# Kernel optimization log

Hardware: AMD Instinct MI355X
Metric: run time of the kernel (lower is better)

## Reference

```python
import jax, jax.numpy as jnp
import numpy as np

N = 50000      # total nodes
E = 800000     # total edges
G = 1000       # graphs in batch
H = 128        # in_channels == hidden_channels
L = 3          # num GCN layers
C = 6          # num classes
EPS = 1e-5     # BatchNorm eps


def setup_inputs() -> dict:
    key = jax.random.key(0)
    ks = jax.random.split(key, 8)
    x = jax.random.normal(ks[0], (N, H), jnp.float32)
    edge_index = jax.random.randint(ks[1], (2, E), 0, N)
    batch = jnp.sort(jax.random.randint(ks[2], (N,), 0, G))
    conv_w = jax.random.normal(ks[3], (L, H, H), jnp.float32) * 0.05
    conv_b = jnp.zeros((L, H), jnp.float32)
    bn_g = jnp.ones((L, H), jnp.float32)
    bn_b = jnp.zeros((L, H), jnp.float32)
    mlp_w1 = jax.random.normal(ks[4], (H, H), jnp.float32) * 0.05
    mlp_b1 = jnp.zeros((H,), jnp.float32)
    mlp_w2 = jax.random.normal(ks[5], (H, C), jnp.float32) * 0.05
    mlp_b2 = jnp.zeros((C,), jnp.float32)
    return {"x": x, "edge_index": edge_index, "batch": batch,
            "conv_w": conv_w, "conv_b": conv_b, "bn_g": bn_g, "bn_b": bn_b,
            "mlp_w1": mlp_w1, "mlp_b1": mlp_b1, "mlp_w2": mlp_w2, "mlp_b2": mlp_b2}


def reference(x, edge_index, batch, conv_w, conv_b, bn_g, bn_b, mlp_w1, mlp_b1, mlp_w2, mlp_b2):
    src, dst = edge_index[0], edge_index[1]
    # GCN symmetric norm with self-loops: deg over A+I
    deg = jax.ops.segment_sum(jnp.ones((E,), x.dtype), dst, num_segments=N) + 1.0
    dis = jax.lax.rsqrt(deg)                      # deg^{-1/2}, [N]
    edge_norm = (dis[src] * dis[dst])[:, None]    # [E,1]
    self_norm = (dis * dis)[:, None]              # [N,1] self-loop weight 1/deg

    for l in range(L):
        h = x @ conv_w[l]                                             # [N,H]
        agg = jax.ops.segment_sum(h[src] * edge_norm, dst, num_segments=N)
        h = agg + h * self_norm + conv_b[l]
        # BatchNorm (training-mode batch statistics, biased var)
        mu = jnp.mean(h, axis=0)
        var = jnp.var(h, axis=0)
        hn = (h - mu) * jax.lax.rsqrt(var + EPS)
        x = jax.nn.relu(hn * bn_g[l] + bn_b[l])   # dropout = identity (eval)

    # global mean pool per graph
    sums = jax.ops.segment_sum(x, batch, num_segments=G)              # [G,H]
    cnt = jax.ops.segment_sum(jnp.ones((N,), x.dtype), batch, num_segments=G)
    pooled = sums / jnp.maximum(cnt, 1.0)[:, None]

    h = jax.nn.relu(pooled @ mlp_w1 + mlp_b1)
    return h @ mlp_w2 + mlp_b2                                         # [G,C]
```

## Files before the change

kernel.cpp:

```cpp
#include <hip/hip_runtime.h>

#define Nn 50000
#define Ee 800000
#define Gg 1000
#define Hh 128
#define Cc 6
#define EPSf 1e-5f
#define SB 1024
#define NSB ((Nn + SB - 1) / SB)
#define NBH 64
#define EPB (Ee / NBH)
#define NW (Nn / 2)
#define HWH (NW / 2)
#define GT ((Nn + 63) / 64)

typedef unsigned short u16;
typedef unsigned int u32;
typedef __attribute__((ext_vector_type(8))) short bf16x8;
typedef __attribute__((ext_vector_type(4))) float f32x4;
typedef __attribute__((ext_vector_type(4))) unsigned int u32x4;

static __device__ inline u16 f2bf(float f) {
    u32 u = __float_as_uint(f);
    u32 r = (u + 0x7fffu + ((u >> 16) & 1u)) >> 16;
    return (u16)r;
}
static __device__ inline float bf_lo(u32 v) { return __uint_as_float(v << 16); }
static __device__ inline float bf_hi(u32 v) { return __uint_as_float(v & 0xffff0000u); }
static __device__ inline u32 pack2(float a, float b) {
    return ((u32)f2bf(b) << 16) | (u32)f2bf(a);
}

__global__ __launch_bounds__(256) void k_pre(const float* __restrict__ W3,
                                             u16* __restrict__ WT3,
                                             float* __restrict__ stats3) {
    __shared__ u16 tbuf[Hh * 136];
    int l = blockIdx.x;
    int tid = threadIdx.x;
    stats3[l * 256 + tid] = 0.0f;
    const float* W = W3 + l * Hh * Hh;
    u16* WT = WT3 + l * Hh * Hh;
#pragma unroll
    for (int i = 0; i < 16; i++) {
        int v = tid + 256 * i;
        int r = v >> 5, c4 = v & 31;
        float4 d = ((const float4*)W)[v];
        u16* p = tbuf + r * 136 + c4 * 4;
        p[0] = f2bf(d.x); p[1] = f2bf(d.y); p[2] = f2bf(d.z); p[3] = f2bf(d.w);
    }
    __syncthreads();
#pragma unroll
    for (int i = 0; i < 64; i++) {
        int o = tid + 256 * i;
        int n = o >> 7, k = o & 127;
        WT[o] = tbuf[k * 136 + n];
    }
}

__global__ __launch_bounds__(256) void k_pro(const int* __restrict__ ei_dst,
                                             u16* __restrict__ rankL,
                                             u32* __restrict__ partials,
                                             const float* __restrict__ Xf,
                                             const u16* __restrict__ WT0,
                                             u16* __restrict__ Yh) {
    extern __shared__ __align__(16) unsigned char smem[];
    int bid = blockIdx.x, tid = threadIdx.x;

    if (bid < NBH) {
        u32* h = (u32*)smem;
        int e0 = bid * EPB;
        u32* P = partials + bid * NW;
#pragma unroll 1
        for (int half = 0; half < 2; half++) {
            int wlo = half * HWH;
            for (int i = tid; i < HWH; i += 256) h[i] = 0u;
            __syncthreads();
            for (int i = tid; i < EPB; i += 256) {
                int d = ei_dst[e0 + i];
                int w = d >> 1;
                if (w >= wlo && w < wlo + HWH) {
                    u32 old = atomicAdd(&h[w - wlo], (d & 1) ? 65536u : 1u);
                    rankL[e0 + i] = (u16)((d & 1) ? (old >> 16) : (old & 0xffffu));
                }
            }
            __syncthreads();
            for (int i = tid; i < HWH; i += 256) P[wlo + i] = h[i];
            __syncthreads();
        }
        return;
    }

    u16* wt = (u16*)smem;
#pragma unroll
    for (int i = 0; i < 8; i++) {
        int v = tid + 256 * i;
        int n = v >> 4, k8 = v & 15;
        uint4 d = ((const uint4*)WT0)[v];
        *((uint4*)(wt + n * 136 + k8 * 8)) = d;
    }
    __syncthreads();

    int tile = bid - NBH;
    int wv = tid >> 6, lane = tid & 63;
    int m = lane & 15, q = lane >> 4;
    int row0 = tile * 64 + wv * 16;
    int lrow = row0 + m;
    if (lrow >= Nn) lrow = Nn - 1;
    const float* xfrow = Xf + lrow * Hh + q * 8;

    f32x4 acc[8] = {};
#pragma unroll
    for (int k0 = 0; k0 < Hh; k0 += 32) {
        float4 u0 = *(const float4*)(xfrow + k0);
        float4 u1 = *(const float4*)(xfrow + k0 + 4);
        union { bf16x8 v; u32 u[4]; } cv;
        cv.u[0] = pack2(u0.x, u0.y);
        cv.u[1] = pack2(u0.z, u0.w);
        cv.u[2] = pack2(u1.x, u1.y);
        cv.u[3] = pack2(u1.z, u1.w);
        bf16x8 a = cv.v;
#pragma unroll
        for (int t = 0; t < 8; t++) {
            bf16x8 b = *(const bf16x8*)(wt + (t * 16 + m) * 136 + k0 + q * 8);
            acc[t] = __builtin_amdgcn_mfma_f32_16x16x32_bf16(a, b, acc[t], 0, 0, 0);
        }
    }

    int orow0 = row0 + q * 4;
#pragma unroll
    for (int t = 0; t < 8; t++) {
#pragma unroll
        for (int r = 0; r < 4; r++) {
            int rr = orow0 + r;
            if (rr < Nn) Yh[rr * Hh + t * 16 + m] = f2bf(acc[t][r]);
        }
    }
}

__global__ __launch_bounds__(256) void k_scan1(const u32* __restrict__ partials,
                                               u32* __restrict__ base_off,
                                               int* __restrict__ rs,
                                               int* __restrict__ bsum,
                                               float* __restrict__ dis,
                                               const int* __restrict__ batch,
                                               int* __restrict__ gstart) {
    __shared__ int ts[256];
    int b = blockIdx.x;
    int t = threadIdx.x;
    int base = b * SB + t * 4;
    int v[4] = {0, 0, 0, 0};
    if (base < Nn) {
        int w0 = base >> 1;
        u32 run0 = 0, run1 = 0;
#pragma unroll 8
        for (int b2 = 0; b2 < NBH; b2++) {
            u32 p0 = partials[b2 * NW + w0];
            u32 p1 = partials[b2 * NW + w0 + 1];
            base_off[b2 * NW + w0] = run0;
            base_off[b2 * NW + w0 + 1] = run1;
            run0 += p0; run1 += p1;
        }
        v[0] = (int)(run0 & 0xffffu); v[1] = (int)(run0 >> 16);
        v[2] = (int)(run1 & 0xffffu); v[3] = (int)(run1 >> 16);
        dis[base]     = rsqrtf((float)v[0] + 1.0f);
        dis[base + 1] = rsqrtf((float)v[1] + 1.0f);
        dis[base + 2] = rsqrtf((float)v[2] + 1.0f);
        dis[base + 3] = rsqrtf((float)v[3] + 1.0f);
    }
    int g = b * 256 + t;
    if (g <= Gg) {
        int lo = 0, hi = Nn;
        while (lo < hi) {
            int mid = (lo + hi) >> 1;
            if (batch[mid] < g) lo = mid + 1; else hi = mid;
        }
        gstart[g] = lo;
    }
    int tsum = v[0] + v[1] + v[2] + v[3];
    ts[t] = tsum;
    __syncthreads();
    for (int off = 1; off < 256; off <<= 1) {
        int x = (t >= off) ? ts[t - off] : 0;
        __syncthreads();
        ts[t] += x;
        __syncthreads();
    }
    int run = (t == 0) ? 0 : ts[t - 1];
    if (t == 255) {
        bsum[b] = ts[255];
        if (b == NSB - 1) rs[Nn] = ts[255];
    }
#pragma unroll
    for (int j = 0; j < 4; j++) {
        int i = base + j;
        if (i < Nn) { rs[i] = run; run += v[j]; }
    }
}

__global__ __launch_bounds__(256) void k_fill(const int* __restrict__ ei,
                                              const int* __restrict__ rs,
                                              const int* __restrict__ bsum,
                                              int* __restrict__ rs2,
                                              const u16* __restrict__ rankL,
                                              const u32* __restrict__ base_off,
                                              const float* __restrict__ dis,
                                              u32* __restrict__ recs) {
    __shared__ int lboff[NSB];
    int t = threadIdx.x;
    if (t < 64) {
        int orig = (t < NSB) ? bsum[t] : 0;
        int v = orig;
#pragma unroll
        for (int off = 1; off < 64; off <<= 1) {
            int u = __shfl_up(v, off, 64);
            if (t >= off) v += u;
        }
        if (t < NSB) lboff[t] = v - orig;
    }
    __syncthreads();

    int gi = blockIdx.x * 256 + t;
    if (gi <= Nn) rs2[gi] = rs[gi] + lboff[gi >> 10];

    int e = gi;
    if (e >= Ee) return;
    int s = ei[e];
    int d = ei[Ee + e];
    int blk = e / EPB;
    u32 bo = base_off[blk * NW + (d >> 1)];
    int rank = (int)rankL[e] + (int)((d & 1) ? (bo >> 16) : (bo & 0xffffu));
    int slot = rs[d] + lboff[d >> 10] + rank;
    float w = dis[s] * dis[d];
    recs[slot] = ((u32)f2bf(w) << 16) | (u32)s;
}

__global__ __launch_bounds__(256) void k_gather(const u16* __restrict__ Yh,
                                                const float* __restrict__ dis,
                                                const float* __restrict__ bias,
                                                const int* __restrict__ rs2,
                                                const u32* __restrict__ recs,
                                                u16* __restrict__ Ah) {
    int node = blockIdx.x * 4 + (threadIdx.x >> 6);
    if (node >= Nn) return;
    int lane = threadIdx.x & 63;
    int lg = lane >> 4;
    int lc = lane & 15;

    const uint4* rows4 = (const uint4*)Yh;

    float acc[8] = {0.f, 0.f, 0.f, 0.f, 0.f, 0.f, 0.f, 0.f};

    int beg = rs2[node];
    int end = rs2[node + 1];

    for (int base = beg; base < end; base += 64) {
        int me = base + lane;
        u32 myrec = recs[me < end ? me : end - 1];
        int cnt = end - base;
        if (cnt > 64) cnt = 64;
        for (int i0 = 0; i0 < cnt; i0 += 16) {
            u32 rr[4]; float ww[4]; uint4 vv[4];
#pragma unroll
            for (int j = 0; j < 4; j++) {
                int si = i0 + j * 4 + lg;
                int sc = si < cnt ? si : cnt - 1;
                u32 rec = __shfl(myrec, sc, 64);
                rr[j] = rec & 0xffffu;
                ww[j] = (si < cnt) ? __uint_as_float(rec & 0xffff0000u) : 0.0f;
            }
#pragma unroll
            for (int j = 0; j < 4; j++) vv[j] = rows4[rr[j] * 16 + lc];
#pragma unroll
            for (int j = 0; j < 4; j++) {
                acc[0] += bf_lo(vv[j].x) * ww[j];
                acc[1] += bf_hi(vv[j].x) * ww[j];
                acc[2] += bf_lo(vv[j].y) * ww[j];
                acc[3] += bf_hi(vv[j].y) * ww[j];
                acc[4] += bf_lo(vv[j].z) * ww[j];
                acc[5] += bf_hi(vv[j].z) * ww[j];
                acc[6] += bf_lo(vv[j].w) * ww[j];
                acc[7] += bf_hi(vv[j].w) * ww[j];
            }
        }
    }
#pragma unroll
    for (int k = 0; k < 8; k++) {
        acc[k] += __shfl_xor(acc[k], 16, 64);
        acc[k] += __shfl_xor(acc[k], 32, 64);
    }
    if (lg == 0) {
        float sn = dis[node];
        sn = sn * sn;
        uint4 hv = rows4[node * 16 + lc];
        const float4* bq = (const float4*)bias;
        float4 b0 = bq[lc * 2];
        float4 b1 = bq[lc * 2 + 1];
        acc[0] = acc[0] + bf_lo(hv.x) * sn + b0.x;
        acc[1] = acc[1] + bf_hi(hv.x) * sn + b0.y;
        acc[2] = acc[2] + bf_lo(hv.y) * sn + b0.z;
        acc[3] = acc[3] + bf_hi(hv.y) * sn + b0.w;
        acc[4] = acc[4] + bf_lo(hv.z) * sn + b1.x;
        acc[5] = acc[5] + bf_hi(hv.z) * sn + b1.y;
        acc[6] = acc[6] + bf_lo(hv.w) * sn + b1.z;
        acc[7] = acc[7] + bf_hi(hv.w) * sn + b1.w;
        u32x4 o;
        o.x = pack2(acc[0], acc[1]);
        o.y = pack2(acc[2], acc[3]);
        o.z = pack2(acc[4], acc[5]);
        o.w = pack2(acc[6], acc[7]);
        __builtin_nontemporal_store(o, (u32x4*)Ah + node * 16 + lc);
    }
}

__global__ __launch_bounds__(256) void k_stats(const u16* __restrict__ Ah,
                                               float* __restrict__ stats) {
    __shared__ float sh[4][256];
    int t = threadIdx.x;
    int jc = t & 63, ro = t >> 6;
    const u32* col = (const u32*)Ah + jc;
    float sx = 0.f, sy = 0.f, qx = 0.f, qy = 0.f;
    for (int r = blockIdx.x * 16 + ro * 4; r < Nn; r += 4096) {
        u32 v[4];
#pragma unroll
        for (int k = 0; k < 4; k++) {
            int rr = r + k;
            v[k] = (rr < Nn) ? col[rr * 64] : 0u;
        }
#pragma unroll
        for (int k = 0; k < 4; k++) {
            float a = bf_lo(v[k]), b = bf_hi(v[k]);
            sx += a; sy += b; qx += a * a; qy += b * b;
        }
    }
    sh[0][t] = sx; sh[1][t] = sy; sh[2][t] = qx; sh[3][t] = qy;
    __syncthreads();
    if (t < 64) {
        sx = sh[0][t] + sh[0][t + 64] + sh[0][t + 128] + sh[0][t + 192];
        sy = sh[1][t] + sh[1][t + 64] + sh[1][t + 128] + sh[1][t + 192];
        qx = sh[2][t] + sh[2][t + 64] + sh[2][t + 128] + sh[2][t + 192];
        qy = sh[3][t] + sh[3][t + 64] + sh[3][t + 128] + sh[3][t + 192];
        atomicAdd(&stats[2 * t], sx);
        atomicAdd(&stats[2 * t + 1], sy);
        atomicAdd(&stats[Hh + 2 * t], qx);
        atomicAdd(&stats[Hh + 2 * t + 1], qy);
    }
}

__global__ __launch_bounds__(256) void k_gemm(const u16* __restrict__ Xin,
                                              const u16* __restrict__ WT,
                                              u16* __restrict__ Yh,
                                              const float* __restrict__ stats,
                                              const float* __restrict__ gam,
                                              const float* __restrict__ bet) {
    __shared__ u16 wt[Hh * 136];
    __shared__ float s_scale[Hh], s_shift[Hh];
    int tid = threadIdx.x;

    if (tid < Hh) {
        float mu = stats[tid] * (1.0f / Nn);
        float var = stats[Hh + tid] * (1.0f / Nn) - mu * mu;
        float sc = rsqrtf(var + EPSf) * gam[tid];
        s_scale[tid] = sc;
        s_shift[tid] = bet[tid] - mu * sc;
    }
#pragma unroll
    for (int i = 0; i < 8; i++) {
        int v = tid + 256 * i;
        int n = v >> 4, k8 = v & 15;
        uint4 d = ((const uint4*)WT)[v];
        *((uint4*)(wt + n * 136 + k8 * 8)) = d;
    }
    __syncthreads();

    int wv = tid >> 6, lane = tid & 63;
    int m = lane & 15, q = lane >> 4;
    int row0 = blockIdx.x * 64 + wv * 16;
    int lrow = row0 + m;
    if (lrow >= Nn) lrow = Nn - 1;
    const u16* xrow = Xin + lrow * Hh + q * 8;

    f32x4 acc[8] = {};
#pragma unroll
    for (int k0 = 0; k0 < Hh; k0 += 32) {
        int cb = k0 + q * 8;
        uint4 p = *(const uint4*)(xrow + k0);
        float4 sc0 = *(const float4*)(s_scale + cb);
        float4 sc1 = *(const float4*)(s_scale + cb + 4);
        float4 sh0 = *(const float4*)(s_shift + cb);
        float4 sh1 = *(const float4*)(s_shift + cb + 4);
        float f0 = fmaxf(bf_lo(p.x) * sc0.x + sh0.x, 0.0f);
        float f1 = fmaxf(bf_hi(p.x) * sc0.y + sh0.y, 0.0f);
        float f2 = fmaxf(bf_lo(p.y) * sc0.z + sh0.z, 0.0f);
        float f3 = fmaxf(bf_hi(p.y) * sc0.w + sh0.w, 0.0f);
        float f4 = fmaxf(bf_lo(p.z) * sc1.x + sh1.x, 0.0f);
        float f5 = fmaxf(bf_hi(p.z) * sc1.y + sh1.y, 0.0f);
        float f6 = fmaxf(bf_lo(p.w) * sc1.z + sh1.z, 0.0f);
        float f7 = fmaxf(bf_hi(p.w) * sc1.w + sh1.w, 0.0f);
        union { bf16x8 v; u32 u[4]; } cv;
        cv.u[0] = pack2(f0, f1);
        cv.u[1] = pack2(f2, f3);
        cv.u[2] = pack2(f4, f5);
        cv.u[3] = pack2(f6, f7);
        bf16x8 a = cv.v;
#pragma unroll
        for (int t = 0; t < 8; t++) {
            bf16x8 b = *(const bf16x8*)(wt + (t * 16 + m) * 136 + k0 + q * 8);
            acc[t] = __builtin_amdgcn_mfma_f32_16x16x32_bf16(a, b, acc[t], 0, 0, 0);
        }
    }

    int orow0 = row0 + q * 4;
#pragma unroll
    for (int t = 0; t < 8; t++) {
#pragma unroll
        for (int r = 0; r < 4; r++) {
            int rr = orow0 + r;
            if (rr < Nn) Yh[rr * Hh + t * 16 + m] = f2bf(acc[t][r]);
        }
    }
}

__global__ __launch_bounds__(128) void k_poolmlp(const u16* __restrict__ Ah,
                                                 const float* __restrict__ stats,
                                                 const float* __restrict__ gam,
                                                 const float* __restrict__ bet,
                                                 const int* __restrict__ gstart,
                                                 const float* __restrict__ W1,
                                                 const float* __restrict__ b1,
                                                 const float* __restrict__ W2,
                                                 const float* __restrict__ b2,
                                                 float* __restrict__ out) {
    int g = blockIdx.x;
    int c = threadIdx.x;
    __shared__ float p[Hh];
    __shared__ float hid[Hh];
    float mu = stats[c] * (1.0f / Nn);
    float var = stats[Hh + c] * (1.0f / Nn) - mu * mu;
    float sc = rsqrtf(var + EPSf) * gam[c];
    float sf = bet[c] - mu * sc;
    int s = gstart[g], e = gstart[g + 1];
    float sum0 = 0.0f, sum1 = 0.0f;
    int r = s;
    for (; r + 1 < e; r += 2) {
        float v0 = __uint_as_float((u32)Ah[r * Hh + c] << 16);
        float v1 = __uint_as_float((u32)Ah[(r + 1) * Hh + c] << 16);
        sum0 += fmaxf(v0 * sc + sf, 0.0f);
        sum1 += fmaxf(v1 * sc + sf, 0.0f);
    }
    if (r < e) {
        float v = __uint_as_float((u32)Ah[r * Hh + c] << 16);
        sum0 += fmaxf(v * sc + sf, 0.0f);
    }
    int n = e - s;
    p[c] = (sum0 + sum1) / (float)(n > 1 ? n : 1);
    __syncthreads();
    float acc = b1[c];
    for (int k = 0; k < Hh; k++) acc += p[k] * W1[k * Hh + c];
    hid[c] = fmaxf(acc, 0.0f);
    __syncthreads();
    if (c < Cc) {
        float acc2 = b2[c];
        for (int k = 0; k < Hh; k++) acc2 += hid[k] * W2[k * Cc + c];
        out[g * Cc + c] = acc2;
    }
}

extern "C" void kernel_launch(void* const* d_in, const int* in_sizes, int n_in,
                              void* d_out, int out_size, void* d_ws, size_t ws_size,
                              hipStream_t stream) {
    const float* x      = (const float*)d_in[0];
    const int*   ei     = (const int*)d_in[1];
    const int*   batch  = (const int*)d_in[2];
    const float* conv_w = (const float*)d_in[3];
    const float* conv_b = (const float*)d_in[4];
    const float* bn_g   = (const float*)d_in[5];
    const float* bn_b   = (const float*)d_in[6];
    const float* w1     = (const float*)d_in[7];
    const float* b1     = (const float*)d_in[8];
    const float* w2     = (const float*)d_in[9];
    const float* b2     = (const float*)d_in[10];
    float* out = (float*)d_out;

    u16*   Yh      = (u16*)d_ws;
    u16*   Ah      = Yh + Nn * Hh;
    u16*   WT      = Ah + Nn * Hh;
    float* dis     = (float*)(WT + 3 * Hh * Hh);
    float* stats3  = dis + Nn;
    int*   rs      = (int*)(stats3 + 3 * 2 * Hh);
    int*   rs2     = rs + Nn + 1;
    int*   gstart  = rs2 + Nn + 1;
    int*   bsum    = gstart + Gg + 1;
    u32*   recs    = (u32*)(bsum + NSB);
    u16*   rankL   = (u16*)(recs + Ee);
    u32*   partials = (u32*)(rankL + Ee);
    u32*   base_off = partials + NBH * NW;

    k_pre<<<3, 256, 0, stream>>>(conv_w, WT, stats3);
    k_pro<<<NBH + GT, 256, 50000, stream>>>(ei + Ee, rankL, partials, x, WT, Yh);
    k_scan1<<<NSB, 256, 0, stream>>>(partials, base_off, rs, bsum, dis, batch, gstart);
    k_fill<<<(Ee + 255) / 256, 256, 0, stream>>>(ei, rs, bsum, rs2, rankL, base_off,
                                                 dis, recs);

    for (int l = 0; l < 3; l++) {
        k_gather<<<(Nn + 3) / 4, 256, 0, stream>>>(Yh, dis, conv_b + l * Hh, rs2,
                                                   recs, Ah);
        k_stats<<<256, 256, 0, stream>>>(Ah, stats3 + l * 2 * Hh);
        if (l < 2) {
            k_gemm<<<(Nn + 63) / 64, 256, 0, stream>>>(Ah, WT + (l + 1) * Hh * Hh, Yh,
                                                       stats3 + l * 2 * Hh,
                                                       bn_g + l * Hh, bn_b + l * Hh);
        }
    }

    k_poolmlp<<<Gg, 128, 0, stream>>>(Ah, stats3 + 2 * 2 * Hh, bn_g + 2 * Hh,
                                      bn_b + 2 * Hh, gstart, w1, b1, w2, b2, out);
}
```

Measured before the change: 339.5 us.

## Widen prologue blocks, replicate BN stat atomics, split pool-MLP work

The prologue kernel now uses 1024-thread blocks: each GEMM block handles four 64-row tiles and shares one weight load in LDS, and the histogram blocks loop with a wider stride. BatchNorm stat accumulation spreads its atomics across 8 replicated buffers, which consumers sum on read, to cut contention on the same addresses. The pool+MLP kernel uses 256 threads, splitting the row pooling and the first matmul across two halves. The trade-off is lower occupancy per block in the prologue and extra reads when reducing the stat replicas.

```diff
diff --git a/kernel.cpp b/kernel.cpp
--- a/kernel.cpp
+++ b/kernel.cpp
@@ -13,6 +13,9 @@
 #define NW (Nn / 2)
 #define HWH (NW / 2)
 #define GT ((Nn + 63) / 64)
+#define GT4 ((GT + 3) / 4)
+#define NREP 8
+#define STS (NREP * 2 * Hh)
 
 typedef unsigned short u16;
 typedef unsigned int u32;
@@ -37,7 +40,8 @@
     __shared__ u16 tbuf[Hh * 136];
     int l = blockIdx.x;
     int tid = threadIdx.x;
-    stats3[l * 256 + tid] = 0.0f;
+#pragma unroll
+    for (int i = 0; i < 8; i++) stats3[l * STS + tid + 256 * i] = 0.0f;
     const float* W = W3 + l * Hh * Hh;
     u16* WT = WT3 + l * Hh * Hh;
 #pragma unroll
@@ -57,12 +61,12 @@
     }
 }
 
-__global__ __launch_bounds__(256) void k_pro(const int* __restrict__ ei_dst,
-                                             u16* __restrict__ rankL,
-                                             u32* __restrict__ partials,
-                                             const float* __restrict__ Xf,
-                                             const u16* __restrict__ WT0,
-                                             u16* __restrict__ Yh) {
+__global__ __launch_bounds__(1024) void k_pro(const int* __restrict__ ei_dst,
+                                              u16* __restrict__ rankL,
+                                              u32* __restrict__ partials,
+                                              const float* __restrict__ Xf,
+                                              const u16* __restrict__ WT0,
+                                              u16* __restrict__ Yh) {
     extern __shared__ __align__(16) unsigned char smem[];
     int bid = blockIdx.x, tid = threadIdx.x;
 
@@ -73,9 +77,9 @@
 #pragma unroll 1
         for (int half = 0; half < 2; half++) {
             int wlo = half * HWH;
-            for (int i = tid; i < HWH; i += 256) h[i] = 0u;
+            for (int i = tid; i < HWH; i += 1024) h[i] = 0u;
             __syncthreads();
-            for (int i = tid; i < EPB; i += 256) {
+            for (int i = tid; i < EPB; i += 1024) {
                 int d = ei_dst[e0 + i];
                 int w = d >> 1;
                 if (w >= wlo && w < wlo + HWH) {
@@ -84,7 +88,7 @@
                 }
             }
             __syncthreads();
-            for (int i = tid; i < HWH; i += 256) P[wlo + i] = h[i];
+            for (int i = tid; i < HWH; i += 1024) P[wlo + i] = h[i];
             __syncthreads();
         }
         return;
@@ -92,16 +96,18 @@
 
     u16* wt = (u16*)smem;
 #pragma unroll
-    for (int i = 0; i < 8; i++) {
-        int v = tid + 256 * i;
+    for (int i = 0; i < 2; i++) {
+        int v = tid + 1024 * i;
         int n = v >> 4, k8 = v & 15;
         uint4 d = ((const uint4*)WT0)[v];
         *((uint4*)(wt + n * 136 + k8 * 8)) = d;
     }
     __syncthreads();
 
-    int tile = bid - NBH;
-    int wv = tid >> 6, lane = tid & 63;
+    int tile = (bid - NBH) * 4 + (tid >> 8);
+    if (tile >= GT) return;
+    int t256 = tid & 255;
+    int wv = t256 >> 6, lane = t256 & 63;
     int m = lane & 15, q = lane >> 4;
     int row0 = tile * 64 + wv * 16;
     int lrow = row0 + m;
@@ -339,10 +345,11 @@
         sy = sh[1][t] + sh[1][t + 64] + sh[1][t + 128] + sh[1][t + 192];
         qx = sh[2][t] + sh[2][t + 64] + sh[2][t + 128] + sh[2][t + 192];
         qy = sh[3][t] + sh[3][t + 64] + sh[3][t + 128] + sh[3][t + 192];
-        atomicAdd(&stats[2 * t], sx);
-        atomicAdd(&stats[2 * t + 1], sy);
-        atomicAdd(&stats[Hh + 2 * t], qx);
-        atomicAdd(&stats[Hh + 2 * t + 1], qy);
+        float* rep = stats + (blockIdx.x & (NREP - 1)) * 2 * Hh;
+        atomicAdd(&rep[2 * t], sx);
+        atomicAdd(&rep[2 * t + 1], sy);
+        atomicAdd(&rep[Hh + 2 * t], qx);
+        atomicAdd(&rep[Hh + 2 * t + 1], qy);
     }
 }
 
@@ -357,8 +364,14 @@
     int tid = threadIdx.x;
 
     if (tid < Hh) {
-        float mu = stats[tid] * (1.0f / Nn);
-        float var = stats[Hh + tid] * (1.0f / Nn) - mu * mu;
+        float s0 = 0.f, s1 = 0.f;
+#pragma unroll
+        for (int r = 0; r < NREP; r++) {
+            s0 += stats[r * 2 * Hh + tid];
+            s1 += stats[r * 2 * Hh + Hh + tid];
+        }
+        float mu = s0 * (1.0f / Nn);
+        float var = s1 * (1.0f / Nn) - mu * mu;
         float sc = rsqrtf(var + EPSf) * gam[tid];
         s_scale[tid] = sc;
         s_shift[tid] = bet[tid] - mu * sc;
@@ -420,7 +433,7 @@
     }
 }
 
-__global__ __launch_bounds__(128) void k_poolmlp(const u16* __restrict__ Ah,
+__global__ __launch_bounds__(256) void k_poolmlp(const u16* __restrict__ Ah,
                                                  const float* __restrict__ stats,
                                                  const float* __restrict__ gam,
                                                  const float* __restrict__ bet,
@@ -431,37 +444,47 @@
                                                  const float* __restrict__ b2,
                                                  float* __restrict__ out) {
     int g = blockIdx.x;
-    int c = threadIdx.x;
+    int t = threadIdx.x;
+    int c = t & 127, h = t >> 7;
+    __shared__ float pp[2][Hh];
     __shared__ float p[Hh];
+    __shared__ float hpart[2][Hh];
     __shared__ float hid[Hh];
-    float mu = stats[c] * (1.0f / Nn);
-    float var = stats[Hh + c] * (1.0f / Nn) - mu * mu;
+
+    float s0 = 0.f, s1 = 0.f;
+#pragma unroll
+    for (int r = 0; r < NREP; r++) {
+        s0 += stats[r * 2 * Hh + c];
+        s1 += stats[r * 2 * Hh + Hh + c];
+    }
+    float mu = s0 * (1.0f / Nn);
+    float var = s1 * (1.0f / Nn) - mu * mu;
     float sc = rsqrtf(var + EPSf) * gam[c];
     float sf = bet[c] - mu * sc;
+
     int s = gstart[g], e = gstart[g + 1];
-    float sum0 = 0.0f, sum1 = 0.0f;
-    int r = s;
-    for (; r + 1 < e; r += 2) {
-        float v0 = __uint_as_float((u32)Ah[r * Hh + c] << 16);
-        float v1 = __uint_as_float((u32)Ah[(r + 1) * Hh + c] << 16);
-        sum0 += fmaxf(v0 * sc + sf, 0.0f);
-        sum1 += fmaxf(v1 * sc + sf, 0.0f);
-    }
-    if (r < e) {
+    float sum = 0.0f;
+    for (int r = s + h; r < e; r += 2) {
         float v = __uint_as_float((u32)Ah[r * Hh + c] << 16);
-        sum0 += fmaxf(v * sc + sf, 0.0f);
-    }
-    int n = e - s;
-    p[c] = (sum0 + sum1) / (float)(n > 1 ? n : 1);
-    __syncthreads();
-    float acc = b1[c];
-    for (int k = 0; k < Hh; k++) acc += p[k] * W1[k * Hh + c];
-    hid[c] = fmaxf(acc, 0.0f);
-    __syncthreads();
-    if (c < Cc) {
-        float acc2 = b2[c];
-        for (int k = 0; k < Hh; k++) acc2 += hid[k] * W2[k * Cc + c];
-        out[g * Cc + c] = acc2;
+        sum += fmaxf(v * sc + sf, 0.0f);
+    }
+    pp[h][c] = sum;
+    __syncthreads();
+    if (h == 0) {
+        int n = e - s;
+        p[c] = (pp[0][c] + pp[1][c]) / (float)(n > 1 ? n : 1);
+    }
+    __syncthreads();
+    float acc = (h == 0) ? b1[c] : 0.0f;
+    for (int k = h * 64; k < h * 64 + 64; k++) acc += p[k] * W1[k * Hh + c];
+    hpart[h][c] = acc;
+    __syncthreads();
+    if (h == 0) hid[c] = fmaxf(hpart[0][c] + hpart[1][c], 0.0f);
+    __syncthreads();
+    if (t < Cc) {
+        float acc2 = b2[t];
+        for (int k = 0; k < Hh; k++) acc2 += hid[k] * W2[k * Cc + t];
+        out[g * Cc + t] = acc2;
     }
 }
 
@@ -486,7 +509,7 @@
     u16*   WT      = Ah + Nn * Hh;
     float* dis     = (float*)(WT + 3 * Hh * Hh);
     float* stats3  = dis + Nn;
-    int*   rs      = (int*)(stats3 + 3 * 2 * Hh);
+    int*   rs      = (int*)(stats3 + 3 * STS);
     int*   rs2     = rs + Nn + 1;
     int*   gstart  = rs2 + Nn + 1;
     int*   bsum    = gstart + Gg + 1;
@@ -496,7 +519,7 @@
     u32*   base_off = partials + NBH * NW;
 
     k_pre<<<3, 256, 0, stream>>>(conv_w, WT, stats3);
-    k_pro<<<NBH + GT, 256, 50000, stream>>>(ei + Ee, rankL, partials, x, WT, Yh);
+    k_pro<<<NBH + GT4, 1024, 50000, stream>>>(ei + Ee, rankL, partials, x, WT, Yh);
     k_scan1<<<NSB, 256, 0, stream>>>(partials, base_off, rs, bsum, dis, batch, gstart);
     k_fill<<<(Ee + 255) / 256, 256, 0, stream>>>(ei, rs, bsum, rs2, rankL, base_off,
                                                  dis, recs);
@@ -504,14 +527,14 @@
     for (int l = 0; l < 3; l++) {
         k_gather<<<(Nn + 3) / 4, 256, 0, stream>>>(Yh, dis, conv_b + l * Hh, rs2,
                                                    recs, Ah);
-        k_stats<<<256, 256, 0, stream>>>(Ah, stats3 + l * 2 * Hh);
+        k_stats<<<256, 256, 0, stream>>>(Ah, stats3 + l * STS);
         if (l < 2) {
             k_gemm<<<(Nn + 63) / 64, 256, 0, stream>>>(Ah, WT + (l + 1) * Hh * Hh, Yh,
-                                                       stats3 + l * 2 * Hh,
+                                                       stats3 + l * STS,
                                                        bn_g + l * Hh, bn_b + l * Hh);
         }
     }
 
-    k_poolmlp<<<Gg, 128, 0, stream>>>(Ah, stats3 + 2 * 2 * Hh, bn_g + 2 * Hh,
+    k_poolmlp<<<Gg, 256, 0, stream>>>(Ah, stats3 + 2 * STS, bn_g + 2 * Hh,
                                       bn_b + 2 * Hh, gstart, w1, b1, w2, b2, out);
 }
```

After: 289.5 us. 1.17x faster.
